# Optimization experiments

Hardware: AMD Instinct MI355X
Metric: run time of the kernel (lower is better)

The kernel has to match this reference:

```python
import jax, jax.numpy as jnp
import numpy as np

EPS = 1e-12  # torch F.normalize eps

def _l2norm(x):
    n = jnp.sqrt(jnp.sum(x * x, axis=-1, keepdims=True))
    return x / jnp.maximum(n, EPS)

def setup_inputs() -> dict:
    key = jax.random.key(0)
    k1, k2 = jax.random.split(key)
    B, C, H, W = 4, 256, 48, 48
    qkv = jax.random.normal(k1, (B, 3 * C, H, W), dtype=jnp.float32)
    temp = jnp.ones((8, 1, 1), dtype=jnp.float32)
    proj_w = jax.random.normal(k2, (C, C), dtype=jnp.float32) * (1.0 / np.sqrt(C))
    proj_b = jnp.zeros((C,), dtype=jnp.float32)
    return {"qkv": qkv, "temp": temp, "proj_w": proj_w, "proj_b": proj_b, "h": H, "w": W}

def reference(qkv, temp, proj_w, proj_b, h, w):
    num_heads = temp.shape[0]
    b = qkv.shape[0]
    q, k, v = jnp.split(qkv, 3, axis=1)

    def to_heads(x):
        # b (head c) h w -> b head (h w) c
        return x.reshape(b, num_heads, -1, h * w).transpose(0, 1, 3, 2)

    q = _l2norm(to_heads(q))
    k = _l2norm(to_heads(k))
    v = to_heads(v)

    # [b, head, N, N], temp (head,1,1) broadcasts over (n, m)
    attn = jnp.einsum('bhnc,bhmc->bhnm', q, k) * temp
    attn = jax.nn.softmax(jax.nn.relu(attn), axis=-1)
    out = jnp.einsum('bhnm,bhmc->bhnc', attn, v)
    # b head N c -> b head c N -> b (head c) h w
    out = out.transpose(0, 1, 3, 2).reshape(b, -1, h, w)
    # 1x1 conv == channel matmul
    out = jnp.einsum('oc,bchw->bohw', proj_w, out) + proj_b[None, :, None, None]
    return out
```

## Files before the change

kernel.cpp:

```cpp
#include <hip/hip_runtime.h>

typedef unsigned short u16;
typedef unsigned int   u32;
typedef __attribute__((ext_vector_type(8))) short short8;
typedef __attribute__((ext_vector_type(4))) float f32x4;

#define NB    4
#define NCH   256
#define NHD   8
#define HD    32
#define NSP   2304
#define NBH   32
#define NKT   36
#define KPW   9

__device__ __forceinline__ u16 f2bf(float f) {
    u32 u = __float_as_uint(f);
    u += 0x7FFFu + ((u >> 16) & 1u);
    return (u16)(u >> 16);
}
__device__ __forceinline__ u32 pack2(float a, float b) {
    return (u32)f2bf(a) | ((u32)f2bf(b) << 16);
}
__device__ __forceinline__ u32 pkfast(float a, float b) {
#if __has_builtin(__builtin_amdgcn_cvt_pk_bf16_f32)
    typedef __attribute__((ext_vector_type(2))) __bf16 bf2;
    union { bf2 v; u32 u; } cv;
    cv.v = __builtin_amdgcn_cvt_pk_bf16_f32(a, b);
    return cv.u;
#else
    return __builtin_amdgcn_perm(__float_as_uint(b), __float_as_uint(a), 0x07060302u);
#endif
}
__device__ __forceinline__ float fexp2(float x) {
#if __has_builtin(__builtin_amdgcn_exp2f)
    return __builtin_amdgcn_exp2f(x);
#else
    return exp2f(x);
#endif
}

__global__ __launch_bounds__(256) void prep_kernel(
    const float* __restrict__ qkv, const float* __restrict__ temp,
    const float* __restrict__ projw,
    u16* __restrict__ Qn, u16* __restrict__ Kn, u16* __restrict__ Vp,
    u16* __restrict__ Wb)
{
    const int p  = blockIdx.y;
    const int bh = blockIdx.z, b = bh >> 3, head = bh & 7;

    if (p == 3) {
        const int idx = (bh * (NSP / 256) + blockIdx.x) * 256 + threadIdx.x;
        if (idx < NCH * NCH / 4) {
            float4 v = ((const float4*)projw)[idx];
            ((uint2*)Wb)[idx] = make_uint2(pack2(v.x, v.y), pack2(v.z, v.w));
        }
        return;
    }

    const int n = blockIdx.x * 256 + threadIdx.x;
    const float* src = qkv + ((size_t)(b * 3 * NCH + p * NCH + head * HD)) * NSP + n;

    float v[HD];
#pragma unroll
    for (int d = 0; d < HD; ++d) v[d] = src[(size_t)d * NSP];

    if (p == 2) {
        const int tile = n >> 6, loc = n & 63;
        const int c = loc >> 5, r5 = loc & 31;
        const int qd  = (r5 < 16) ? (r5 >> 2) : ((r5 - 16) >> 2);
        const int jj  = (r5 < 16) ? (r5 & 3) : (4 + (r5 & 3));
        u16* dst = Vp + (size_t)bh * NSP * HD + (size_t)tile * 2048 + c * 32 + qd * 8 + jj;
#pragma unroll
        for (int d = 0; d < HD; ++d) dst[d * 64] = f2bf(v[d]);
    } else {
        float s = 0.f;
#pragma unroll
        for (int d = 0; d < HD; ++d) s += v[d] * v[d];
        float sc = 1.f / fmaxf(sqrtf(s), 1e-12f);
        if (p == 0) sc *= temp[head] * 1.44269504088896f;
        u32 pk[HD / 2];
#pragma unroll
        for (int i = 0; i < HD / 2; ++i) pk[i] = pack2(v[2 * i] * sc, v[2 * i + 1] * sc);
        u16* dst = (p == 0 ? Qn : Kn) + ((size_t)bh * NSP + n) * HD;
#pragma unroll
        for (int i = 0; i < 4; ++i) ((uint4*)dst)[i] = ((const uint4*)pk)[i];
    }
}

__global__ __launch_bounds__(256) void attn_kernel(
    const u16* __restrict__ Qn, const u16* __restrict__ Kn,
    const u16* __restrict__ Vp, u16* __restrict__ X)
{
    __shared__ float cmb[4][64][49];
    const int bh = blockIdx.x, b = bh >> 3, head = bh & 7;
    const int w = threadIdx.x >> 6, lane = threadIdx.x & 63;
    const int l15 = lane & 15, quad = lane >> 4;
    const int qbase = blockIdx.y * 64;

    const u16* Kg = Kn + (size_t)bh * NSP * HD + (size_t)w * KPW * 2048 + l15 * HD + quad * 8;
    const u16* Vg = Vp + (size_t)bh * NSP * HD + (size_t)w * KPW * 2048 + l15 * 64 + quad * 8;

    short8 qf[4];
#pragma unroll
    for (int t2 = 0; t2 < 4; ++t2)
        qf[t2] = *(const short8*)(Qn + ((size_t)bh * NSP + qbase + t2 * 16 + l15) * HD + quad * 8);

    const short one = (short)0x3F80;
    const short8 vones = {one, one, one, one, one, one, one, one};

    f32x4 oacc[4][2] = {{{0,0,0,0},{0,0,0,0}},{{0,0,0,0},{0,0,0,0}},
                        {{0,0,0,0},{0,0,0,0}},{{0,0,0,0},{0,0,0,0}}};
    f32x4 rsac[4]    = {{0,0,0,0},{0,0,0,0},{0,0,0,0},{0,0,0,0}};

    short8 ka[4];
#pragma unroll
    for (int i = 0; i < 4; ++i) ka[i] = *(const short8*)(Kg + i * 512);

    for (int kt = 0; kt < KPW; ++kt) {
        short8 vb[2][2];
#pragma unroll
        for (int c = 0; c < 2; ++c)
#pragma unroll
            for (int h = 0; h < 2; ++h)
                vb[c][h] = *(const short8*)(Vg + (size_t)kt * 2048 + h * 1024 + c * 32);
        short8 kan[4];
        if (kt + 1 < KPW) {
            const u16* Kp2 = Kg + (size_t)(kt + 1) * 2048;
#pragma unroll
            for (int i = 0; i < 4; ++i) kan[i] = *(const short8*)(Kp2 + i * 512);
        }

#pragma unroll
        for (int t2 = 0; t2 < 4; ++t2) {
            f32x4 sf[4];
#pragma unroll
            for (int i = 0; i < 4; ++i)
                sf[i] = __builtin_amdgcn_mfma_f32_16x16x32_bf16(ka[i], qf[t2], (f32x4){0.f,0.f,0.f,0.f}, 0, 0, 0);
            u32 pk[4][2];
#pragma unroll
            for (int i = 0; i < 4; ++i) {
                pk[i][0] = pkfast(fexp2(fmaxf(sf[i][0], 0.f)), fexp2(fmaxf(sf[i][1], 0.f)));
                pk[i][1] = pkfast(fexp2(fmaxf(sf[i][2], 0.f)), fexp2(fmaxf(sf[i][3], 0.f)));
            }
#pragma unroll
            for (int c = 0; c < 2; ++c) {
                union { short8 s; u32 u[4]; } pa;
                pa.u[0] = pk[2 * c][0];     pa.u[1] = pk[2 * c][1];
                pa.u[2] = pk[2 * c + 1][0]; pa.u[3] = pk[2 * c + 1][1];
                oacc[t2][0] = __builtin_amdgcn_mfma_f32_16x16x32_bf16(pa.s, vb[c][0], oacc[t2][0], 0, 0, 0);
                oacc[t2][1] = __builtin_amdgcn_mfma_f32_16x16x32_bf16(pa.s, vb[c][1], oacc[t2][1], 0, 0, 0);
                rsac[t2]    = __builtin_amdgcn_mfma_f32_16x16x32_bf16(pa.s, vones,    rsac[t2],    0, 0, 0);
            }
        }

        if (kt + 1 < KPW) {
#pragma unroll
            for (int i = 0; i < 4; ++i) ka[i] = kan[i];
        }
    }

    {
        float* my = &cmb[w][lane][0];
#pragma unroll
        for (int t2 = 0; t2 < 4; ++t2) {
#pragma unroll
            for (int h = 0; h < 2; ++h)
#pragma unroll
                for (int r = 0; r < 4; ++r) my[t2 * 12 + h * 4 + r] = oacc[t2][h][r];
#pragma unroll
            for (int r = 0; r < 4; ++r) my[t2 * 12 + 8 + r] = rsac[t2][r];
        }
    }
    __syncthreads();
    {
        const int t2 = w;
        float o0[4] = {0,0,0,0}, o1[4] = {0,0,0,0}, rsum[4] = {0,0,0,0};
#pragma unroll
        for (int j = 0; j < 4; ++j) {
            const float* srcp = &cmb[j][lane][t2 * 12];
#pragma unroll
            for (int r = 0; r < 4; ++r) {
                o0[r]   += srcp[r];
                o1[r]   += srcp[4 + r];
                rsum[r] += srcp[8 + r];
            }
        }
        u16* Xb = X + (size_t)b * NSP * NCH + head * HD;
#pragma unroll
        for (int r = 0; r < 4; ++r) {
            const float inv = 1.f / rsum[r];
            u16* row = Xb + (size_t)(qbase + t2 * 16 + quad * 4 + r) * NCH;
            row[l15]      = f2bf(o0[r] * inv);
            row[16 + l15] = f2bf(o1[r] * inv);
        }
    }
}

__global__ __launch_bounds__(64) void proj_kernel(
    const u16* __restrict__ Wb, const u16* __restrict__ X,
    const float* __restrict__ bias, float* __restrict__ out)
{
    const int b = blockIdx.z;
    const int lane = threadIdx.x;
    const int l15 = lane & 15, quad = lane >> 4;
    const int obase = blockIdx.y * 16;
    const int nbase = blockIdx.x * 32;

    const u16* wrow = Wb + (size_t)(obase + l15) * NCH + quad * 8;
    const u16* xrow = X + ((size_t)b * NSP + nbase + l15) * NCH + quad * 8;

    f32x4 acc[2] = {{0,0,0,0},{0,0,0,0}};
#pragma unroll
    for (int ks = 0; ks < 8; ++ks) {
        const short8 af = *(const short8*)(wrow + ks * 32);
        acc[0] = __builtin_amdgcn_mfma_f32_16x16x32_bf16(af, *(const short8*)(xrow + ks * 32), acc[0], 0, 0, 0);
        acc[1] = __builtin_amdgcn_mfma_f32_16x16x32_bf16(af, *(const short8*)(xrow + (size_t)16 * NCH + ks * 32), acc[1], 0, 0, 0);
    }
#pragma unroll
    for (int r = 0; r < 4; ++r) {
        const int o = obase + quad * 4 + r;
        const float bo = bias[o];
        float* orow = out + ((size_t)b * NCH + o) * NSP + nbase;
        orow[l15]      = acc[0][r] + bo;
        orow[16 + l15] = acc[1][r] + bo;
    }
}

extern "C" void kernel_launch(void* const* d_in, const int* in_sizes, int n_in,
                              void* d_out, int out_size, void* d_ws, size_t ws_size,
                              hipStream_t stream) {
    const float* qkv   = (const float*)d_in[0];
    const float* temp  = (const float*)d_in[1];
    const float* projw = (const float*)d_in[2];
    const float* projb = (const float*)d_in[3];
    float* out = (float*)d_out;

    u16* Qn = (u16*)d_ws;
    u16* Kn = Qn + (size_t)NBH * NSP * HD;
    u16* Vp = Kn + (size_t)NBH * NSP * HD;
    u16* X  = Vp + (size_t)NBH * NSP * HD;
    u16* Wb = X + (size_t)NB * NSP * NCH;

    prep_kernel<<<dim3(NSP / 256, 4, NBH), dim3(256), 0, stream>>>(qkv, temp, projw, Qn, Kn, Vp, Wb);
    attn_kernel<<<dim3(NBH, NSP / 64), dim3(256), 0, stream>>>(Qn, Kn, Vp, X);
    proj_kernel<<<dim3(NSP / 32, NCH / 16, NB), dim3(64), 0, stream>>>(Wb, X, projb, out);
}
```

Before: 149.9 us.

## Vectorize prep to two pixels per thread, halve attn LDS, widen proj blocks

The prep kernel now handles two spatial positions per thread, using float2 loads and packed 32-bit V stores on a 192-thread grid. The attention kernel's cross-wave reduction buffer is halved by running it in two passes with an extra barrier, and launch bounds request 4 blocks per CU, aiming at higher occupancy. The projection kernel uses 4 waves per block covering 64 output channels instead of single-wave blocks, which cuts launch and scheduling overhead. The trade-offs are more registers per thread in prep and an additional sync in the attention epilogue.

```diff
diff --git a/kernel.cpp b/kernel.cpp
--- a/kernel.cpp
+++ b/kernel.cpp
@@ -40,7 +40,7 @@
 #endif
 }
 
-__global__ __launch_bounds__(256) void prep_kernel(
+__global__ __launch_bounds__(192) void prep_kernel(
     const float* __restrict__ qkv, const float* __restrict__ temp,
     const float* __restrict__ projw,
     u16* __restrict__ Qn, u16* __restrict__ Kn, u16* __restrict__ Vp,
@@ -50,7 +50,7 @@
     const int bh = blockIdx.z, b = bh >> 3, head = bh & 7;
 
     if (p == 3) {
-        const int idx = (bh * (NSP / 256) + blockIdx.x) * 256 + threadIdx.x;
+        const int idx = (bh * 6 + blockIdx.x) * 192 + threadIdx.x;
         if (idx < NCH * NCH / 4) {
             float4 v = ((const float4*)projw)[idx];
             ((uint2*)Wb)[idx] = make_uint2(pack2(v.x, v.y), pack2(v.z, v.w));
@@ -58,41 +58,48 @@
         return;
     }
 
-    const int n = blockIdx.x * 256 + threadIdx.x;
-    const float* src = qkv + ((size_t)(b * 3 * NCH + p * NCH + head * HD)) * NSP + n;
-
-    float v[HD];
-#pragma unroll
-    for (int d = 0; d < HD; ++d) v[d] = src[(size_t)d * NSP];
+    const int i  = blockIdx.x * 192 + threadIdx.x;
+    const int n0 = i * 2;
+    const float* src = qkv + ((size_t)(b * 3 * NCH + p * NCH + head * HD)) * NSP + n0;
+
+    float2 v[HD];
+#pragma unroll
+    for (int d = 0; d < HD; ++d) v[d] = *(const float2*)(src + (size_t)d * NSP);
 
     if (p == 2) {
-        const int tile = n >> 6, loc = n & 63;
+        const int tile = n0 >> 6, loc = n0 & 63;
         const int c = loc >> 5, r5 = loc & 31;
         const int qd  = (r5 < 16) ? (r5 >> 2) : ((r5 - 16) >> 2);
         const int jj  = (r5 < 16) ? (r5 & 3) : (4 + (r5 & 3));
         u16* dst = Vp + (size_t)bh * NSP * HD + (size_t)tile * 2048 + c * 32 + qd * 8 + jj;
 #pragma unroll
-        for (int d = 0; d < HD; ++d) dst[d * 64] = f2bf(v[d]);
+        for (int d = 0; d < HD; ++d) *(u32*)(dst + d * 64) = pack2(v[d].x, v[d].y);
     } else {
-        float s = 0.f;
-#pragma unroll
-        for (int d = 0; d < HD; ++d) s += v[d] * v[d];
-        float sc = 1.f / fmaxf(sqrtf(s), 1e-12f);
-        if (p == 0) sc *= temp[head] * 1.44269504088896f;
-        u32 pk[HD / 2];
-#pragma unroll
-        for (int i = 0; i < HD / 2; ++i) pk[i] = pack2(v[2 * i] * sc, v[2 * i + 1] * sc);
-        u16* dst = (p == 0 ? Qn : Kn) + ((size_t)bh * NSP + n) * HD;
-#pragma unroll
-        for (int i = 0; i < 4; ++i) ((uint4*)dst)[i] = ((const uint4*)pk)[i];
-    }
-}
-
-__global__ __launch_bounds__(256) void attn_kernel(
+        float s0 = 0.f, s1 = 0.f;
+#pragma unroll
+        for (int d = 0; d < HD; ++d) { s0 += v[d].x * v[d].x; s1 += v[d].y * v[d].y; }
+        float sc0 = 1.f / fmaxf(sqrtf(s0), 1e-12f);
+        float sc1 = 1.f / fmaxf(sqrtf(s1), 1e-12f);
+        if (p == 0) {
+            const float t = temp[head] * 1.44269504088896f;
+            sc0 *= t; sc1 *= t;
+        }
+        u32 pk[HD];
+#pragma unroll
+        for (int j = 0; j < HD / 2; ++j) pk[j]          = pack2(v[2 * j].x * sc0, v[2 * j + 1].x * sc0);
+#pragma unroll
+        for (int j = 0; j < HD / 2; ++j) pk[HD / 2 + j] = pack2(v[2 * j].y * sc1, v[2 * j + 1].y * sc1);
+        u16* dst = (p == 0 ? Qn : Kn) + ((size_t)bh * NSP + n0) * HD;
+#pragma unroll
+        for (int j = 0; j < 8; ++j) ((uint4*)dst)[j] = ((const uint4*)pk)[j];
+    }
+}
+
+__global__ __launch_bounds__(256, 4) void attn_kernel(
     const u16* __restrict__ Qn, const u16* __restrict__ Kn,
     const u16* __restrict__ Vp, u16* __restrict__ X)
 {
-    __shared__ float cmb[4][64][49];
+    __shared__ float cmb[4][64][25];
     const int bh = blockIdx.x, b = bh >> 3, head = bh & 7;
     const int w = threadIdx.x >> 6, lane = threadIdx.x & 63;
     const int l15 = lane & 15, quad = lane >> 4;
@@ -108,6 +115,7 @@
 
     const short one = (short)0x3F80;
     const short8 vones = {one, one, one, one, one, one, one, one};
+    const f32x4 zf = {0.f, 0.f, 0.f, 0.f};
 
     f32x4 oacc[4][2] = {{{0,0,0,0},{0,0,0,0}},{{0,0,0,0},{0,0,0,0}},
                         {{0,0,0,0},{0,0,0,0}},{{0,0,0,0},{0,0,0,0}}};
@@ -136,7 +144,7 @@
             f32x4 sf[4];
 #pragma unroll
             for (int i = 0; i < 4; ++i)
-                sf[i] = __builtin_amdgcn_mfma_f32_16x16x32_bf16(ka[i], qf[t2], (f32x4){0.f,0.f,0.f,0.f}, 0, 0, 0);
+                sf[i] = __builtin_amdgcn_mfma_f32_16x16x32_bf16(ka[i], qf[t2], zf, 0, 0, 0);
             u32 pk[4][2];
 #pragma unroll
             for (int i = 0; i < 4; ++i) {
@@ -160,51 +168,57 @@
         }
     }
 
-    {
-        float* my = &cmb[w][lane][0];
-#pragma unroll
-        for (int t2 = 0; t2 < 4; ++t2) {
-#pragma unroll
-            for (int h = 0; h < 2; ++h)
-#pragma unroll
-                for (int r = 0; r < 4; ++r) my[t2 * 12 + h * 4 + r] = oacc[t2][h][r];
-#pragma unroll
-            for (int r = 0; r < 4; ++r) my[t2 * 12 + 8 + r] = rsac[t2][r];
-        }
-    }
-    __syncthreads();
-    {
-        const int t2 = w;
-        float o0[4] = {0,0,0,0}, o1[4] = {0,0,0,0}, rsum[4] = {0,0,0,0};
-#pragma unroll
-        for (int j = 0; j < 4; ++j) {
-            const float* srcp = &cmb[j][lane][t2 * 12];
+#pragma unroll
+    for (int pass = 0; pass < 2; ++pass) {
+        if (pass) __syncthreads();
+        {
+            float* my = &cmb[w][lane][0];
+#pragma unroll
+            for (int tt = 0; tt < 2; ++tt) {
+                const int t2 = pass * 2 + tt;
+#pragma unroll
+                for (int h = 0; h < 2; ++h)
+#pragma unroll
+                    for (int r = 0; r < 4; ++r) my[tt * 12 + h * 4 + r] = oacc[t2][h][r];
+#pragma unroll
+                for (int r = 0; r < 4; ++r) my[tt * 12 + 8 + r] = rsac[t2][r];
+            }
+        }
+        __syncthreads();
+        if ((w >> 1) == pass) {
+            const int t2 = w;
+            const int tt = w & 1;
+            float o0[4] = {0,0,0,0}, o1[4] = {0,0,0,0}, rsum[4] = {0,0,0,0};
+#pragma unroll
+            for (int j = 0; j < 4; ++j) {
+                const float* srcp = &cmb[j][lane][tt * 12];
+#pragma unroll
+                for (int r = 0; r < 4; ++r) {
+                    o0[r]   += srcp[r];
+                    o1[r]   += srcp[4 + r];
+                    rsum[r] += srcp[8 + r];
+                }
+            }
+            u16* Xb = X + (size_t)b * NSP * NCH + head * HD;
 #pragma unroll
             for (int r = 0; r < 4; ++r) {
-                o0[r]   += srcp[r];
-                o1[r]   += srcp[4 + r];
-                rsum[r] += srcp[8 + r];
-            }
-        }
-        u16* Xb = X + (size_t)b * NSP * NCH + head * HD;
-#pragma unroll
-        for (int r = 0; r < 4; ++r) {
-            const float inv = 1.f / rsum[r];
-            u16* row = Xb + (size_t)(qbase + t2 * 16 + quad * 4 + r) * NCH;
-            row[l15]      = f2bf(o0[r] * inv);
-            row[16 + l15] = f2bf(o1[r] * inv);
-        }
-    }
-}
-
-__global__ __launch_bounds__(64) void proj_kernel(
+                const float inv = 1.f / rsum[r];
+                u16* row = Xb + (size_t)(qbase + t2 * 16 + quad * 4 + r) * NCH;
+                row[l15]      = f2bf(o0[r] * inv);
+                row[16 + l15] = f2bf(o1[r] * inv);
+            }
+        }
+    }
+}
+
+__global__ __launch_bounds__(256) void proj_kernel(
     const u16* __restrict__ Wb, const u16* __restrict__ X,
     const float* __restrict__ bias, float* __restrict__ out)
 {
     const int b = blockIdx.z;
-    const int lane = threadIdx.x;
+    const int w = threadIdx.x >> 6, lane = threadIdx.x & 63;
     const int l15 = lane & 15, quad = lane >> 4;
-    const int obase = blockIdx.y * 16;
+    const int obase = blockIdx.y * 64 + w * 16;
     const int nbase = blockIdx.x * 32;
 
     const u16* wrow = Wb + (size_t)(obase + l15) * NCH + quad * 8;
@@ -242,7 +256,7 @@
     u16* X  = Vp + (size_t)NBH * NSP * HD;
     u16* Wb = X + (size_t)NB * NSP * NCH;
 
-    prep_kernel<<<dim3(NSP / 256, 4, NBH), dim3(256), 0, stream>>>(qkv, temp, projw, Qn, Kn, Vp, Wb);
+    prep_kernel<<<dim3(6, 4, NBH), dim3(192), 0, stream>>>(qkv, temp, projw, Qn, Kn, Vp, Wb);
     attn_kernel<<<dim3(NBH, NSP / 64), dim3(256), 0, stream>>>(Qn, Kn, Vp, X);
-    proj_kernel<<<dim3(NSP / 32, NCH / 16, NB), dim3(64), 0, stream>>>(Wb, X, projb, out);
-}
+    proj_kernel<<<dim3(NSP / 32, NCH / 64, NB), dim3(256), 0, stream>>>(Wb, X, projb, out);
+}
```

Result: slower. 163.3 us (+8.9%).
